# Kernel tuning notes

Measured on AMD Instinct MI355X. Metric: run time of the kernel, lower is better.

The kernel has to match this reference:

```python
import jax, jax.numpy as jnp
import numpy as np

N_LAYERS = 2          # number of (Dense, Erf) pairs before final Dense
PI = np.float32(np.pi)
EPS = np.float32(1e-7)


def setup_inputs() -> dict:
    key = jax.random.key(0)
    kx, ky = jax.random.split(key)
    x = jax.random.normal(kx, (8192, 512), dtype=jnp.float32)
    y = jax.random.normal(ky, (8192, 512), dtype=jnp.float32)
    return {"x": x, "y": y}


def _erf_diag(c):
    # E[erf(u)^2] for u ~ N(0, c):  (2/pi) * arcsin(2c / (1 + 2c))
    return (2.0 / PI) * jnp.arcsin(2.0 * c / (1.0 + 2.0 * c))


def reference(x, y):
    d = x.shape[1]
    inv_d = jnp.float32(1.0 / d)
    # First Dense (W_std=1, no bias): nngp = x.y^T / d, ntk = nngp
    nngp = (x @ y.T) * inv_d                      # [n, m]
    cx = jnp.sum(x * x, axis=1) * inv_d           # [n] diagonal second moments
    cy = jnp.sum(y * y, axis=1) * inv_d           # [m]
    ntk = nngp
    for _ in range(N_LAYERS):
        # Erf nonlinearity (analytic arcsine kernel)
        prod = (1.0 + 2.0 * cx)[:, None] * (1.0 + 2.0 * cy)[None, :]  # [n, m]
        ratio = jnp.clip(2.0 * nngp * jax.lax.rsqrt(prod), -1.0 + EPS, 1.0 - EPS)
        nngp_new = (2.0 / PI) * jnp.arcsin(ratio)
        dot = (4.0 / PI) * jax.lax.rsqrt(jnp.maximum(prod - 4.0 * nngp * nngp, EPS))
        ntk = ntk * dot
        nngp = nngp_new
        cx = _erf_diag(cx)
        cy = _erf_diag(cy)
        # Dense (W_std=1, no bias): nngp unchanged, ntk += nngp
        ntk = ntk + nngp
    return ntk  # kernel_type == 'ntk'
```

## Files before the change

kernel.cpp:

```cpp
#include <hip/hip_runtime.h>
#include <hip/hip_bf16.h>
#include <math.h>

#define D_K  512
#define NROW 8192
#define BM   128
#define BN   128
#define BK   64

typedef __attribute__((ext_vector_type(8))) short bf16x8;
typedef __attribute__((ext_vector_type(4))) float f32x4;

#if __has_builtin(__builtin_amdgcn_rsqf)
#define RSQ(x) __builtin_amdgcn_rsqf(x)
#else
#define RSQ(x) rsqrtf(x)
#endif

__device__ __forceinline__ unsigned short f2bf(float f) {
    unsigned int u = __float_as_uint(f);
    unsigned int r = (u + 0x7FFFu + ((u >> 16) & 1u)) >> 16;
    return (unsigned short)r;
}

__device__ __forceinline__ void load_lds16(const unsigned short* g, unsigned short* l) {
    __builtin_amdgcn_global_load_lds(
        (const __attribute__((address_space(1))) unsigned int*)g,
        (__attribute__((address_space(3))) unsigned int*)l,
        16, 0, 0);
}

__global__ void prep_kernel(const float* __restrict__ xin, const float* __restrict__ yin,
                            unsigned short* __restrict__ xb, unsigned short* __restrict__ yb,
                            float* __restrict__ px0, float* __restrict__ px1,
                            float* __restrict__ py0, float* __restrict__ py1)
{
    const int row   = blockIdx.x;
    const int which = blockIdx.y;
    const float* src = (which ? yin : xin) + (size_t)row * D_K;
    unsigned short* dst = (which ? yb : xb) + (size_t)row * D_K;
    const int t = threadIdx.x;

    float2 v = ((const float2*)src)[t];
    ushort2 b; b.x = f2bf(v.x); b.y = f2bf(v.y);
    ((ushort2*)dst)[t] = b;

    float s = v.x * v.x + v.y * v.y;
    for (int o = 32; o > 0; o >>= 1) s += __shfl_down(s, o, 64);
    __shared__ float red[4];
    if ((t & 63) == 0) red[t >> 6] = s;
    __syncthreads();
    if (t == 0) {
        float tot = red[0] + red[1] + red[2] + red[3];
        float c0 = tot * (1.0f / D_K);
        float a0 = 1.0f + 2.0f * c0;
        float c1 = 0.636619772367581343f * asinf(2.0f * c0 / a0);
        float a1 = 1.0f + 2.0f * c1;
        if (which) {
            py0[row] = 1.0f / sqrtf(a0);
            py1[row] = 1.0f / sqrtf(a1);
        } else {
            px0[row] = 2.0f / sqrtf(a0);
            px1[row] = 2.0f / sqrtf(a1);
        }
    }
}

__device__ __forceinline__ void layer_step(float& nngp, float& ntk, float s) {
    float ratio = nngp * s;
    ratio = fminf(fmaxf(ratio, -0.9999999f), 0.9999999f);
    float u = ratio * ratio;
    float p = fmaf(u, 0.011046346f, 0.014241648f);
    p = fmaf(u, p, 0.019340246f);
    p = fmaf(u, p, 0.028420525f);
    p = fmaf(u, p, 0.047746483f);
    p = fmaf(u, p, 0.106103295f);
    p = fmaf(u, p, 0.636619772f);
    float nngp_new = ratio * p;
    float rv = RSQ(1.0f - u);
    float dot = 0.636619772f * (s * rv);
    ntk = fmaf(ntk, dot, nngp_new);
    nngp = nngp_new;
}

__global__ void ntk_kernel(const unsigned short* __restrict__ xb,
                           const unsigned short* __restrict__ yb,
                           const float* __restrict__ px0, const float* __restrict__ px1,
                           const float* __restrict__ py0, const float* __restrict__ py1,
                           float* __restrict__ out)
{
    __shared__ unsigned short As[BM * BK];
    __shared__ unsigned short Bs[BN * BK];

    const int tid  = threadIdx.x;
    const int lane = tid & 63;
    const int wid  = tid >> 6;
    const int wr   = wid >> 1;
    const int wc   = wid & 1;
    const int rowBase = blockIdx.y * BM;
    const int colBase = blockIdx.x * BN;
    const int l15 = lane & 15;
    const int lg  = lane >> 4;

    f32x4 acc[4][4];
    #pragma unroll
    for (int m = 0; m < 4; m++)
        #pragma unroll
        for (int n = 0; n < 4; n++)
            acc[m][n] = (f32x4){0.f, 0.f, 0.f, 0.f};

    for (int ks = 0; ks < D_K; ks += BK) {
        __syncthreads();
        #pragma unroll
        for (int r = 0; r < 4; r++) {
            int base = r * 256 + wid * 64;
            int idx  = base + lane;
            int row  = idx >> 3;
            int c    = (idx & 7) ^ (row & 7);
            const unsigned short* gA = xb + (size_t)(rowBase + row) * D_K + ks + c * 8;
            load_lds16(gA, &As[base * 8]);
            const unsigned short* gB = yb + (size_t)(colBase + row) * D_K + ks + c * 8;
            load_lds16(gB, &Bs[base * 8]);
        }
        __syncthreads();

        bf16x8 af[2][4], bfr[2][4];
        #pragma unroll
        for (int s = 0; s < 2; s++) {
            #pragma unroll
            for (int m = 0; m < 4; m++) {
                int rowA = wr * 64 + m * 16 + l15;
                int slA  = ((s * 4 + lg) ^ (rowA & 7)) * 8;
                af[s][m] = *(const bf16x8*)&As[rowA * BK + slA];
                int rowB = wc * 64 + m * 16 + l15;
                int slB  = ((s * 4 + lg) ^ (rowB & 7)) * 8;
                bfr[s][m] = *(const bf16x8*)&Bs[rowB * BK + slB];
            }
        }
        #pragma unroll
        for (int s = 0; s < 2; s++)
            #pragma unroll
            for (int m = 0; m < 4; m++)
                #pragma unroll
                for (int n = 0; n < 4; n++)
                    acc[m][n] = __builtin_amdgcn_mfma_f32_16x16x32_bf16(
                        af[s][m], bfr[s][n], acc[m][n], 0, 0, 0);
    }

    float py0v[4], py1v[4];
    int   colv[4];
    #pragma unroll
    for (int n = 0; n < 4; n++) {
        int col = colBase + wc * 64 + n * 16 + l15;
        colv[n] = col;
        py0v[n] = py0[col];
        py1v[n] = py1[col];
    }
    #pragma unroll
    for (int m = 0; m < 4; m++) {
        int row0 = rowBase + wr * 64 + m * 16 + lg * 4;
        #pragma unroll
        for (int j = 0; j < 4; j++) {
            int row = row0 + j;
            float a0 = px0[row], a1 = px1[row];
            #pragma unroll
            for (int n = 0; n < 4; n++) {
                float nngp = acc[m][n][j] * (1.0f / D_K);
                float ntk = nngp;
                layer_step(nngp, ntk, a0 * py0v[n]);
                layer_step(nngp, ntk, a1 * py1v[n]);
                out[(size_t)row * NROW + colv[n]] = ntk;
            }
        }
    }
}

extern "C" void kernel_launch(void* const* d_in, const int* in_sizes, int n_in,
                              void* d_out, int out_size, void* d_ws, size_t ws_size,
                              hipStream_t stream)
{
    const float* x = (const float*)d_in[0];
    const float* y = (const float*)d_in[1];
    float* out = (float*)d_out;

    char* ws = (char*)d_ws;
    unsigned short* xb = (unsigned short*)ws;
    unsigned short* yb = (unsigned short*)(ws + (size_t)8 * 1024 * 1024);
    float* px0 = (float*)(ws + (size_t)16 * 1024 * 1024);
    float* px1 = px0 + NROW;
    float* py0 = px1 + NROW;
    float* py1 = py0 + NROW;

    dim3 pgrid(NROW, 2);
    prep_kernel<<<pgrid, 256, 0, stream>>>(x, y, xb, yb, px0, px1, py0, py1);

    dim3 grid(NROW / BN, NROW / BM);
    ntk_kernel<<<grid, 256, 0, stream>>>(xb, yb, px0, px1, py0, py1, out);
}
```

Before: 136.2 us.

## Use 256x256 tiles with double-buffered LDS pipeline and block swizzle

Grows the output tile to 256x256 with 512 threads (8 waves, 2x4) and double-buffers LDS in K halves, so global-to-LDS loads for the next K step overlap the MFMAs on the current one. It uses manual s_waitcnt and s_barrier with s_setprio around the MFMA bursts, and remaps block IDs with a swizzle for L2 locality. It also drops the fast rsq builtin in favour of rsqrtf. The aim is to cut load latency stalls and redundant global traffic in the GEMM, but it adds register pressure from 128 accumulator floats per lane and depends on hand-counted vmcnt values being correct.

```diff
diff --git a/kernel.cpp b/kernel.cpp
--- a/kernel.cpp
+++ b/kernel.cpp
@@ -4,18 +4,16 @@
 
 #define D_K  512
 #define NROW 8192
-#define BM   128
-#define BN   128
+#define BM   256
+#define BN   256
 #define BK   64
+#define NT   (D_K / BK)
 
 typedef __attribute__((ext_vector_type(8))) short bf16x8;
 typedef __attribute__((ext_vector_type(4))) float f32x4;
 
-#if __has_builtin(__builtin_amdgcn_rsqf)
-#define RSQ(x) __builtin_amdgcn_rsqf(x)
-#else
-#define RSQ(x) rsqrtf(x)
-#endif
+#define BAR()    asm volatile("s_barrier" ::: "memory")
+#define WAITV4() asm volatile("s_waitcnt vmcnt(4)" ::: "memory")
 
 __device__ __forceinline__ unsigned short f2bf(float f) {
     unsigned int u = __float_as_uint(f);
@@ -77,74 +75,135 @@
     p = fmaf(u, p, 0.106103295f);
     p = fmaf(u, p, 0.636619772f);
     float nngp_new = ratio * p;
-    float rv = RSQ(1.0f - u);
+    float rv = rsqrtf(1.0f - u);
     float dot = 0.636619772f * (s * rv);
     ntk = fmaf(ntk, dot, nngp_new);
     nngp = nngp_new;
 }
 
-__global__ void ntk_kernel(const unsigned short* __restrict__ xb,
-                           const unsigned short* __restrict__ yb,
-                           const float* __restrict__ px0, const float* __restrict__ px1,
-                           const float* __restrict__ py0, const float* __restrict__ py1,
-                           float* __restrict__ out)
+__device__ __forceinline__ void stage_half(const unsigned short* __restrict__ gbase,
+                                           unsigned short* lhalf, int ks_col,
+                                           int tid, int wid, int lane) {
+    #pragma unroll
+    for (int l = 0; l < 2; l++) {
+        int idx = l * 512 + tid;
+        int row = idx >> 2;
+        int c   = (idx & 3) ^ ((row >> 1) & 3);
+        const unsigned short* g = gbase + (size_t)row * D_K + ks_col + c * 8;
+        load_lds16(g, lhalf + (size_t)(l * 512 + wid * 64) * 8);
+    }
+}
+
+__device__ __forceinline__ void read_frags4(const unsigned short* half_, bf16x8* fr,
+                                            int rbase, int l15, int lg) {
+    #pragma unroll
+    for (int i = 0; i < 4; i++) {
+        int row = rbase + i * 16 + l15;
+        int sl  = lg ^ ((row >> 1) & 3);
+        fr[i] = *(const bf16x8*)&half_[row * 32 + sl * 8];
+    }
+}
+
+__global__ void __launch_bounds__(512, 2)
+ntk_kernel(const unsigned short* __restrict__ xb,
+           const unsigned short* __restrict__ yb,
+           const float* __restrict__ px0, const float* __restrict__ px1,
+           const float* __restrict__ py0, const float* __restrict__ py1,
+           float* __restrict__ out)
 {
-    __shared__ unsigned short As[BM * BK];
-    __shared__ unsigned short Bs[BN * BK];
+    __shared__ unsigned short lds[2][2][2][256 * 32];
 
     const int tid  = threadIdx.x;
     const int lane = tid & 63;
     const int wid  = tid >> 6;
-    const int wr   = wid >> 1;
-    const int wc   = wid & 1;
-    const int rowBase = blockIdx.y * BM;
-    const int colBase = blockIdx.x * BN;
-    const int l15 = lane & 15;
-    const int lg  = lane >> 4;
-
-    f32x4 acc[4][4];
-    #pragma unroll
-    for (int m = 0; m < 4; m++)
+    const int wr   = wid >> 2;
+    const int wc   = wid & 3;
+    const int l15  = lane & 15;
+    const int lg   = lane >> 4;
+
+    const int bid = blockIdx.x;
+    const int swz = (bid & 7) * 128 + (bid >> 3);
+    const int bx  = swz & 31;
+    const int by  = swz >> 5;
+    const int rowBase = by * BM;
+    const int colBase = bx * BN;
+
+    const unsigned short* gA = xb + (size_t)rowBase * D_K;
+    const unsigned short* gB = yb + (size_t)colBase * D_K;
+
+    f32x4 acc[8][4];
+    #pragma unroll
+    for (int m = 0; m < 8; m++)
         #pragma unroll
         for (int n = 0; n < 4; n++)
             acc[m][n] = (f32x4){0.f, 0.f, 0.f, 0.f};
 
-    for (int ks = 0; ks < D_K; ks += BK) {
-        __syncthreads();
-        #pragma unroll
-        for (int r = 0; r < 4; r++) {
-            int base = r * 256 + wid * 64;
-            int idx  = base + lane;
-            int row  = idx >> 3;
-            int c    = (idx & 7) ^ (row & 7);
-            const unsigned short* gA = xb + (size_t)(rowBase + row) * D_K + ks + c * 8;
-            load_lds16(gA, &As[base * 8]);
-            const unsigned short* gB = yb + (size_t)(colBase + row) * D_K + ks + c * 8;
-            load_lds16(gB, &Bs[base * 8]);
-        }
-        __syncthreads();
-
-        bf16x8 af[2][4], bfr[2][4];
-        #pragma unroll
-        for (int s = 0; s < 2; s++) {
-            #pragma unroll
-            for (int m = 0; m < 4; m++) {
-                int rowA = wr * 64 + m * 16 + l15;
-                int slA  = ((s * 4 + lg) ^ (rowA & 7)) * 8;
-                af[s][m] = *(const bf16x8*)&As[rowA * BK + slA];
-                int rowB = wc * 64 + m * 16 + l15;
-                int slB  = ((s * 4 + lg) ^ (rowB & 7)) * 8;
-                bfr[s][m] = *(const bf16x8*)&Bs[rowB * BK + slB];
-            }
-        }
-        #pragma unroll
-        for (int s = 0; s < 2; s++)
-            #pragma unroll
-            for (int m = 0; m < 4; m++)
-                #pragma unroll
-                for (int n = 0; n < 4; n++)
-                    acc[m][n] = __builtin_amdgcn_mfma_f32_16x16x32_bf16(
-                        af[s][m], bfr[s][n], acc[m][n], 0, 0, 0);
+    bf16x8 af[4], bf[4];
+
+    stage_half(gA, &lds[0][0][0][0], 0,  tid, wid, lane);
+    stage_half(gB, &lds[0][1][0][0], 0,  tid, wid, lane);
+    stage_half(gA, &lds[0][0][1][0], 32, tid, wid, lane);
+    stage_half(gB, &lds[0][1][1][0], 32, tid, wid, lane);
+    WAITV4();
+    BAR();
+
+    #pragma unroll 2
+    for (int kt = 0; kt < NT; kt++) {
+        const int buf  = kt & 1;
+        const int bufN = buf ^ 1;
+        const int ksn  = ((kt + 1) * BK) & (D_K - 1);
+
+        read_frags4(&lds[buf][0][0][0], af, wr * 128 + 0,  l15, lg);
+        read_frags4(&lds[buf][1][0][0], bf, wc * 64,       l15, lg);
+        stage_half(gA, &lds[bufN][0][0][0], ksn, tid, wid, lane);
+        BAR();
+        __builtin_amdgcn_s_setprio(1);
+        #pragma unroll
+        for (int m = 0; m < 4; m++)
+            #pragma unroll
+            for (int n = 0; n < 4; n++)
+                acc[m][n] = __builtin_amdgcn_mfma_f32_16x16x32_bf16(af[m], bf[n], acc[m][n], 0, 0, 0);
+        __builtin_amdgcn_s_setprio(0);
+        BAR();
+
+        read_frags4(&lds[buf][0][0][0], af, wr * 128 + 64, l15, lg);
+        stage_half(gB, &lds[bufN][1][0][0], ksn, tid, wid, lane);
+        BAR();
+        __builtin_amdgcn_s_setprio(1);
+        #pragma unroll
+        for (int m = 0; m < 4; m++)
+            #pragma unroll
+            for (int n = 0; n < 4; n++)
+                acc[4 + m][n] = __builtin_amdgcn_mfma_f32_16x16x32_bf16(af[m], bf[n], acc[4 + m][n], 0, 0, 0);
+        __builtin_amdgcn_s_setprio(0);
+        WAITV4();
+        BAR();
+
+        read_frags4(&lds[buf][0][1][0], af, wr * 128 + 0,  l15, lg);
+        read_frags4(&lds[buf][1][1][0], bf, wc * 64,       l15, lg);
+        stage_half(gA, &lds[bufN][0][1][0], ksn + 32, tid, wid, lane);
+        BAR();
+        __builtin_amdgcn_s_setprio(1);
+        #pragma unroll
+        for (int m = 0; m < 4; m++)
+            #pragma unroll
+            for (int n = 0; n < 4; n++)
+                acc[m][n] = __builtin_amdgcn_mfma_f32_16x16x32_bf16(af[m], bf[n], acc[m][n], 0, 0, 0);
+        __builtin_amdgcn_s_setprio(0);
+        BAR();
+
+        read_frags4(&lds[buf][0][1][0], af, wr * 128 + 64, l15, lg);
+        stage_half(gB, &lds[bufN][1][1][0], ksn + 32, tid, wid, lane);
+        BAR();
+        __builtin_amdgcn_s_setprio(1);
+        #pragma unroll
+        for (int m = 0; m < 4; m++)
+            #pragma unroll
+            for (int n = 0; n < 4; n++)
+                acc[4 + m][n] = __builtin_amdgcn_mfma_f32_16x16x32_bf16(af[m], bf[n], acc[4 + m][n], 0, 0, 0);
+        __builtin_amdgcn_s_setprio(0);
+        WAITV4();
+        BAR();
     }
 
     float py0v[4], py1v[4];
@@ -157,8 +216,8 @@
         py1v[n] = py1[col];
     }
     #pragma unroll
-    for (int m = 0; m < 4; m++) {
-        int row0 = rowBase + wr * 64 + m * 16 + lg * 4;
+    for (int m = 0; m < 8; m++) {
+        int row0 = rowBase + wr * 128 + m * 16 + lg * 4;
         #pragma unroll
         for (int j = 0; j < 4; j++) {
             int row = row0 + j;
@@ -194,6 +253,5 @@
     dim3 pgrid(NROW, 2);
     prep_kernel<<<pgrid, 256, 0, stream>>>(x, y, xb, yb, px0, px1, py0, py1);
 
-    dim3 grid(NROW / BN, NROW / BM);
-    ntk_kernel<<<grid, 256, 0, stream>>>(xb, yb, px0, px1, py0, py1, out);
-}
+    ntk_kernel<<<(NROW / BM) * (NROW / BN), 512, 0, stream>>>(xb, yb, px0, px1, py0, py1, out);
+}
```

Result: slower. 169.3 us (+24.3%).
